# Performance work log

Measured on AMD Instinct MI355X. Metric: run time of the kernel, lower is better.

Reference implementation:

```python
import jax, jax.numpy as jnp
import numpy as np

N_Z = 128
N_COMP = 10
N_CLASSES = 10
BS = 8192


def setup_inputs() -> dict:
    key = jax.random.key(0)
    k_z, k_g, k_m = jax.random.split(key, 3)
    z = jax.random.normal(k_z, (BS, N_Z), dtype=jnp.float32)
    y = jax.random.randint(k_g, (BS,), 0, N_CLASSES, dtype=jnp.int64)
    # Gumbel noise replicating torch F.gumbel_softmax internal sampling
    gumbel = jax.random.gumbel(jax.random.fold_in(key, 1), (N_CLASSES, BS, N_COMP), dtype=jnp.float32)
    m = jax.random.normal(k_m, (N_CLASSES, N_COMP, N_Z), dtype=jnp.float32)
    # torch init: L = eye(n_z) per (class, component)
    L = jnp.broadcast_to(jnp.eye(N_Z, dtype=jnp.float32), (N_CLASSES, N_COMP, N_Z, N_Z))
    logits = jnp.zeros((N_CLASSES, N_COMP), dtype=jnp.float32)
    return {"z": z, "y": y, "gumbel": gumbel, "m": m, "L": L, "logits": logits}


def reference(z, y, gumbel, m, L, logits):
    C, K = logits.shape
    # hard gumbel-softmax (tau=1) per class, straight-through
    scores = logits[:, None, :] + gumbel                 # (C, bs, K)
    soft = jax.nn.softmax(scores, axis=-1)               # (C, bs, K)
    hard = jax.nn.one_hot(jnp.argmax(scores, axis=-1), K, dtype=soft.dtype)
    comp_mask = hard + soft - jax.lax.stop_gradient(soft)  # (C, bs, K)
    # every class/component affine: m + z @ L.T -> (C, K, bs, n_z)
    samps = jnp.einsum('bi,ckji->ckbj', z, L) + m[:, :, None, :]
    # select component per (class, sample)
    per_class = jnp.einsum('cbk,ckbj->cbj', comp_mask, samps)  # (C, bs, n_z)
    # select class per sample via one-hot(y)
    y1h = jax.nn.one_hot(y, C, dtype=per_class.dtype)          # (bs, C)
    x = jnp.einsum('bc,cbj->bj', y1h, per_class)               # (bs, n_z)
    return x
```

## Files before the change

kernel.cpp:

```cpp
#include <hip/hip_runtime.h>


#define N_Z 128
#define N_COMP 10
#define N_CLASSES 10
#define N_CK (N_CLASSES * N_COMP)
#define TB 56
#define ZPITCH 132
#define LIST_CAP 256

__global__ __launch_bounds__(64) void k_select(
    const int* __restrict__ y, const float* __restrict__ gumbel,
    const float* __restrict__ logits, unsigned char* __restrict__ ck_arr, int bs)
{
    int b = blockIdx.x * 64 + threadIdx.x;
    if (b >= bs) return;
    int c = y[b];
    const float* g  = gumbel + ((size_t)c * bs + b) * N_COMP;
    const float* lg = logits + c * N_COMP;
    float best = g[0] + lg[0];
    int bi = 0;
    #pragma unroll
    for (int k = 1; k < N_COMP; ++k) {
        float s = g[k] + lg[k];
        if (s > best) { best = s; bi = k; }
    }
    ck_arr[b] = (unsigned char)(c * N_COMP + bi);
}

__global__ __launch_bounds__(256) void k_gemm(
    const float* __restrict__ z, const float* __restrict__ m,
    const float* __restrict__ L, const unsigned char* __restrict__ ck_arr,
    float* __restrict__ out, int bs)
{
    const int ck = blockIdx.x;
    const int jh = blockIdx.y;
    const int bh = blockIdx.z;

    __shared__ __align__(16) float Ls[64 * 128];
    __shared__ __align__(16) float zs[TB * ZPITCH];
    __shared__ int list[LIST_CAP];
    __shared__ int cnt;

    const int t = threadIdx.x;
    if (t == 0) cnt = 0;

    {
        const float4* Lg4 = (const float4*)(L + ((size_t)ck * N_Z + jh * 64) * N_Z);
        #pragma unroll
        for (int p = 0; p < 8; ++p) {
            int f  = p * 256 + t;
            int jl = f >> 5;
            int fi = f & 31;
            float4 v = Lg4[f];
            int col = ((fi << 2) + 4 * jl) & 127;
            *(float4*)&Ls[jl * 128 + col] = v;
        }
    }
    __syncthreads();

    {
        const int half = bs >> 1;
        const uint4* ck4 = (const uint4*)(ck_arr + bh * half);
        int idx = t;
        uint4 v = ck4[idx];
        int b0 = bh * half + idx * 16;
        unsigned w[4] = {v.x, v.y, v.z, v.w};
        #pragma unroll
        for (int q = 0; q < 4; ++q) {
            #pragma unroll
            for (int e = 0; e < 4; ++e) {
                if (((w[q] >> (8 * e)) & 0xFFu) == (unsigned)ck) {
                    int p2 = atomicAdd(&cnt, 1);
                    if (p2 < LIST_CAP) list[p2] = b0 + q * 4 + e;
                }
            }
        }
    }
    __syncthreads();

    const int n = min(cnt, LIST_CAP);

    const int jg  = t & 15;
    const int sg  = t >> 4;
    const int sl4 = sg << 2;

    for (int s0 = 0; s0 < n; s0 += TB) {
        const int ns = min(TB, n - s0);

        #pragma unroll
        for (int p = 0; p < 7; ++p) {
            int f  = p * 256 + t;
            int sl = f >> 5;
            int fi = f & 31;
            int samp = list[s0 + (sl < ns ? sl : 0)];
            float4 v = *(const float4*)(z + (size_t)samp * N_Z + fi * 4);
            *(float4*)&zs[sl * ZPITCH + fi * 4] = v;
        }
        __syncthreads();

        if (sl4 < ns) {
            float acc[4][4] = {};
            #pragma unroll 2
            for (int i = 0; i < N_Z; i += 4) {
                float4 zv[4];
                #pragma unroll
                for (int s = 0; s < 4; ++s)
                    zv[s] = *(const float4*)&zs[(sl4 + s) * ZPITCH + i];
                #pragma unroll
                for (int r = 0; r < 4; ++r) {
                    int jl  = jg + 16 * r;
                    int col = (i + 4 * jl) & 127;
                    float4 lv = *(const float4*)&Ls[jl * 128 + col];
                    acc[r][0] += lv.x * zv[0].x + lv.y * zv[0].y + lv.z * zv[0].z + lv.w * zv[0].w;
                    acc[r][1] += lv.x * zv[1].x + lv.y * zv[1].y + lv.z * zv[1].z + lv.w * zv[1].w;
                    acc[r][2] += lv.x * zv[2].x + lv.y * zv[2].y + lv.z * zv[2].z + lv.w * zv[2].w;
                    acc[r][3] += lv.x * zv[3].x + lv.y * zv[3].y + lv.z * zv[3].z + lv.w * zv[3].w;
                }
            }
            #pragma unroll
            for (int r = 0; r < 4; ++r) {
                int j = jh * 64 + jg + 16 * r;
                float mm = m[ck * N_Z + j];
                #pragma unroll
                for (int s = 0; s < 4; ++s) {
                    int sl = sl4 + s;
                    if (sl < ns) {
                        int samp = list[s0 + sl];
                        out[(size_t)samp * N_Z + j] = acc[r][s] + mm;
                    }
                }
            }
        }
        __syncthreads();
    }
}

extern "C" void kernel_launch(void* const* d_in, const int* in_sizes, int n_in,
                              void* d_out, int out_size, void* d_ws, size_t ws_size,
                              hipStream_t stream)
{
    const float* z      = (const float*)d_in[0];
    const int*   y      = (const int*)d_in[1];
    const float* gumbel = (const float*)d_in[2];
    const float* m      = (const float*)d_in[3];
    const float* L      = (const float*)d_in[4];
    const float* logits = (const float*)d_in[5];
    float* out = (float*)d_out;

    const int bs = in_sizes[0] / N_Z;

    unsigned char* ck_arr = (unsigned char*)d_ws;

    k_select<<<(bs + 63) / 64, 64, 0, stream>>>(y, gumbel, logits, ck_arr, bs);
    k_gemm<<<dim3(N_CK, 2, 2), 256, 0, stream>>>(z, m, L, ck_arr, out, bs);
}
```

Baseline: 90.53 us.

## Use bf16 MFMA for per-component affine and drop batch-half grid split

Converts L and gathered z rows to bf16 in shared memory and computes the per-sample affine transform with 16x16x32 bf16 MFMA instructions instead of scalar FP32 dot products. Each block now scans the whole batch's component assignments rather than half, halving the grid and removing duplicate L loads. This cuts ALU work and LDS traffic, at the cost of bf16 rounding error in the output and less grid parallelism. The LDS layout of L is no longer swizzled, which can cause bank conflicts.

Result: faster. 84.83 us (-6.3%).

```diff
diff --git a/kernel.cpp b/kernel.cpp
--- a/kernel.cpp
+++ b/kernel.cpp
@@ -5,9 +5,12 @@
 #define N_COMP 10
 #define N_CLASSES 10
 #define N_CK (N_CLASSES * N_COMP)
-#define TB 56
-#define ZPITCH 132
+#define ZCAP 96
 #define LIST_CAP 256
+
+typedef __attribute__((ext_vector_type(4))) __bf16 bf16x4;
+typedef __attribute__((ext_vector_type(8))) __bf16 bf16x8;
+typedef __attribute__((ext_vector_type(4))) float f32x4;
 
 __global__ __launch_bounds__(64) void k_select(
     const int* __restrict__ y, const float* __restrict__ gumbel,
@@ -28,17 +31,16 @@
     ck_arr[b] = (unsigned char)(c * N_COMP + bi);
 }
 
-__global__ __launch_bounds__(256) void k_gemm(
+__global__ __launch_bounds__(256) void k_mfma(
     const float* __restrict__ z, const float* __restrict__ m,
     const float* __restrict__ L, const unsigned char* __restrict__ ck_arr,
     float* __restrict__ out, int bs)
 {
     const int ck = blockIdx.x;
     const int jh = blockIdx.y;
-    const int bh = blockIdx.z;
 
-    __shared__ __align__(16) float Ls[64 * 128];
-    __shared__ __align__(16) float zs[TB * ZPITCH];
+    __shared__ __align__(16) __bf16 Lsb[64 * 128];
+    __shared__ __align__(16) __bf16 zsb[ZCAP * 128];
     __shared__ int list[LIST_CAP];
     __shared__ int cnt;
 
@@ -49,30 +51,30 @@
         const float4* Lg4 = (const float4*)(L + ((size_t)ck * N_Z + jh * 64) * N_Z);
         #pragma unroll
         for (int p = 0; p < 8; ++p) {
-            int f  = p * 256 + t;
-            int jl = f >> 5;
-            int fi = f & 31;
+            int f = p * 256 + t;
             float4 v = Lg4[f];
-            int col = ((fi << 2) + 4 * jl) & 127;
-            *(float4*)&Ls[jl * 128 + col] = v;
+            bf16x4 b4 = { (__bf16)v.x, (__bf16)v.y, (__bf16)v.z, (__bf16)v.w };
+            *(bf16x4*)&Lsb[f * 4] = b4;
         }
     }
     __syncthreads();
 
     {
-        const int half = bs >> 1;
-        const uint4* ck4 = (const uint4*)(ck_arr + bh * half);
-        int idx = t;
-        uint4 v = ck4[idx];
-        int b0 = bh * half + idx * 16;
-        unsigned w[4] = {v.x, v.y, v.z, v.w};
+        const uint4* ck4 = (const uint4*)ck_arr;
         #pragma unroll
-        for (int q = 0; q < 4; ++q) {
+        for (int p = 0; p < 2; ++p) {
+            int idx = p * 256 + t;
+            uint4 v = ck4[idx];
+            int b0 = idx * 16;
+            unsigned w[4] = {v.x, v.y, v.z, v.w};
             #pragma unroll
-            for (int e = 0; e < 4; ++e) {
-                if (((w[q] >> (8 * e)) & 0xFFu) == (unsigned)ck) {
-                    int p2 = atomicAdd(&cnt, 1);
-                    if (p2 < LIST_CAP) list[p2] = b0 + q * 4 + e;
+            for (int q = 0; q < 4; ++q) {
+                #pragma unroll
+                for (int e = 0; e < 4; ++e) {
+                    if (((w[q] >> (8 * e)) & 0xFFu) == (unsigned)ck) {
+                        int p2 = atomicAdd(&cnt, 1);
+                        if (p2 < LIST_CAP) list[p2] = b0 + q * 4 + e;
+                    }
                 }
             }
         }
@@ -81,54 +83,59 @@
 
     const int n = min(cnt, LIST_CAP);
 
-    const int jg  = t & 15;
-    const int sg  = t >> 4;
-    const int sl4 = sg << 2;
+    const int wv   = t >> 6;
+    const int lane = t & 63;
+    const int mn   = lane & 15;
+    const int quad = lane >> 4;
 
-    for (int s0 = 0; s0 < n; s0 += TB) {
-        const int ns = min(TB, n - s0);
+    for (int s0 = 0; s0 < n; s0 += ZCAP) {
+        const int ns = min(ZCAP, n - s0);
 
         #pragma unroll
-        for (int p = 0; p < 7; ++p) {
-            int f  = p * 256 + t;
-            int sl = f >> 5;
-            int fi = f & 31;
-            int samp = list[s0 + (sl < ns ? sl : 0)];
-            float4 v = *(const float4*)(z + (size_t)samp * N_Z + fi * 4);
-            *(float4*)&zs[sl * ZPITCH + fi * 4] = v;
+        for (int p = 0; p < 12; ++p) {
+            int f   = p * 256 + t;
+            int row = f >> 5;
+            if (row < ns) {
+                int samp = list[s0 + row];
+                float4 v = *(const float4*)(z + (size_t)samp * N_Z + (f & 31) * 4);
+                bf16x4 b4 = { (__bf16)v.x, (__bf16)v.y, (__bf16)v.z, (__bf16)v.w };
+                *(bf16x4*)&zsb[row * 128 + (f & 31) * 4] = b4;
+            }
         }
         __syncthreads();
 
-        if (sl4 < ns) {
-            float acc[4][4] = {};
-            #pragma unroll 2
-            for (int i = 0; i < N_Z; i += 4) {
-                float4 zv[4];
+        const int ntiles = (ns + 15) >> 4;
+        #pragma unroll
+        for (int half = 0; half < 2; ++half) {
+            int nt = wv + half * 4;
+            if (nt >= ntiles) break;
+            int nb = nt * 16;
+            int srow = nb + mn;
+
+            bf16x8 bf[4];
+            #pragma unroll
+            for (int ks = 0; ks < 4; ++ks)
+                bf[ks] = *(const bf16x8*)&zsb[srow * 128 + ks * 32 + quad * 8];
+
+            #pragma unroll
+            for (int mt = 0; mt < 4; ++mt) {
+                f32x4 acc = {0.f, 0.f, 0.f, 0.f};
                 #pragma unroll
-                for (int s = 0; s < 4; ++s)
-                    zv[s] = *(const float4*)&zs[(sl4 + s) * ZPITCH + i];
-                #pragma unroll
-                for (int r = 0; r < 4; ++r) {
-                    int jl  = jg + 16 * r;
-                    int col = (i + 4 * jl) & 127;
-                    float4 lv = *(const float4*)&Ls[jl * 128 + col];
-                    acc[r][0] += lv.x * zv[0].x + lv.y * zv[0].y + lv.z * zv[0].z + lv.w * zv[0].w;
-                    acc[r][1] += lv.x * zv[1].x + lv.y * zv[1].y + lv.z * zv[1].z + lv.w * zv[1].w;
-                    acc[r][2] += lv.x * zv[2].x + lv.y * zv[2].y + lv.z * zv[2].z + lv.w * zv[2].w;
-                    acc[r][3] += lv.x * zv[3].x + lv.y * zv[3].y + lv.z * zv[3].z + lv.w * zv[3].w;
+                for (int ks = 0; ks < 4; ++ks) {
+                    bf16x8 af = *(const bf16x8*)&Lsb[(mt * 16 + mn) * 128 + ks * 32 + quad * 8];
+                    acc = __builtin_amdgcn_mfma_f32_16x16x32_bf16(af, bf[ks], acc, 0, 0, 0);
                 }
-            }
-            #pragma unroll
-            for (int r = 0; r < 4; ++r) {
-                int j = jh * 64 + jg + 16 * r;
-                float mm = m[ck * N_Z + j];
-                #pragma unroll
-                for (int s = 0; s < 4; ++s) {
-                    int sl = sl4 + s;
-                    if (sl < ns) {
-                        int samp = list[s0 + sl];
-                        out[(size_t)samp * N_Z + j] = acc[r][s] + mm;
-                    }
+                int sidx = nb + mn;
+                if (sidx < ns) {
+                    int samp = list[s0 + sidx];
+                    int j0 = jh * 64 + mt * 16 + quad * 4;
+                    float4 mv = *(const float4*)(m + ck * N_Z + j0);
+                    float4 o;
+                    o.x = acc.x + mv.x;
+                    o.y = acc.y + mv.y;
+                    o.z = acc.z + mv.z;
+                    o.w = acc.w + mv.w;
+                    *(float4*)(out + (size_t)samp * N_Z + j0) = o;
                 }
             }
         }
@@ -153,5 +160,5 @@
     unsigned char* ck_arr = (unsigned char*)d_ws;
 
     k_select<<<(bs + 63) / 64, 64, 0, stream>>>(y, gumbel, logits, ck_arr, bs);
-    k_gemm<<<dim3(N_CK, 2, 2), 256, 0, stream>>>(z, m, L, ck_arr, out, bs);
+    k_mfma<<<dim3(N_CK, 2), 256, 0, stream>>>(z, m, L, ck_arr, out, bs);
 }
```
